# Optimization experiments

Hardware: AMD Instinct MI355X
Metric: run time of the kernel (lower is better)

## Reference

```python
import jax, jax.numpy as jnp
import numpy as np

DIM = 172
MULT = 4
HEADS = 1
B, H, W = 2, 256, 256


def _ln(x, g, b):
    # LayerNorm over last dim, eps=1e-5 (torch default)
    m = jnp.mean(x, axis=-1, keepdims=True)
    v = jnp.mean((x - m) ** 2, axis=-1, keepdims=True)
    return (x - m) * jax.lax.rsqrt(v + 1e-5) * g + b


def _l2norm(x):
    # F.normalize(p=2, dim=-1): x / max(||x||, 1e-12)
    n = jnp.sqrt(jnp.sum(x * x, axis=-1, keepdims=True))
    return x / jnp.maximum(n, 1e-12)


def _gelu(x):
    return jax.nn.gelu(x, approximate=False)


def _dwconv3(x, w):
    # x: [B,C,H,W], w: [C,1,3,3], groups=C, padding=1
    return jax.lax.conv_general_dilated(
        x, w, window_strides=(1, 1), padding='SAME',
        feature_group_count=x.shape[1],
        dimension_numbers=('NCHW', 'OIHW', 'NCHW'))


def _c1x1(x, w):
    # 1x1 conv, no bias. x: [B,I,H,W], w: [O,I,1,1]
    return jnp.einsum('bihw,oi->bohw', x, w[:, :, 0, 0])


def _ms_msa(x, Wq, Wk, Wv, rescale, proj_w, proj_b, pos_w1, pos_w2):
    # x: [b,h,w,c] (already layer-normed)
    b, h, w, c = x.shape
    d = c // HEADS
    n = h * w
    xf = x.reshape(b, n, c)
    q_inp = xf @ Wq.T
    k_inp = xf @ Wk.T
    v_inp = xf @ Wv.T

    def split(t):  # -> [b, heads, d, n]  (b n (h d) -> b h n d, then transpose(-2,-1))
        return t.reshape(b, n, HEADS, d).transpose(0, 2, 3, 1)

    q, k, v = split(q_inp), split(k_inp), split(v_inp)
    q = _l2norm(q)
    k = _l2norm(k)
    attn = jnp.einsum('bhdn,bhen->bhde', k, q)  # k @ q^T -> [b,heads,d,d]
    attn = attn * rescale                        # learnable per-head rescale
    attn = jax.nn.softmax(attn, axis=-1)
    xo = jnp.einsum('bhde,bhen->bhdn', attn, v)  # [b,heads,d,n]
    xo = xo.transpose(0, 3, 1, 2).reshape(b, n, HEADS * d)
    out_c = (xo @ proj_w.T + proj_b).reshape(b, h, w, c)
    # residual positional embedding: depthwise conv -> GELU -> depthwise conv on v_inp
    vim = v_inp.reshape(b, h, w, c).transpose(0, 3, 1, 2)
    out_p = _dwconv3(_gelu(_dwconv3(vim, pos_w1)), pos_w2).transpose(0, 2, 3, 1)
    return out_c + out_p


def _ffn(x, w1, dw, w2):
    # FeedForward: 1x1 expand -> GELU -> 3x3 depthwise -> GELU -> 1x1 project
    y = x.transpose(0, 3, 1, 2)
    y = _gelu(_c1x1(y, w1))
    y = _gelu(_dwconv3(y, dw))
    y = _c1x1(y, w2)
    return y.transpose(0, 2, 3, 1)


def reference(x, ln1_g, ln1_b, Wq, Wk, Wv, rescale, proj_w, proj_b,
              pos_w1, pos_w2, ln2_g, ln2_b, ff_w1, ff_dw, ff_w2):
    # SMSAB forward, num_blocks=1. x: [b,c,h,w]
    y = x.transpose(0, 2, 3, 1)  # [b,h,w,c]
    y = _ms_msa(_ln(y, ln1_g, ln1_b), Wq, Wk, Wv, rescale,
                proj_w, proj_b, pos_w1, pos_w2) + y
    y = _ffn(_ln(y, ln2_g, ln2_b), ff_w1, ff_dw, ff_w2) + y
    return y.transpose(0, 3, 1, 2)  # [b,c,h,w]


def setup_inputs() -> dict:
    key = jax.random.key(0)
    ks = jax.random.split(key, 9)
    s = 0.02
    c, m = DIM, DIM * MULT
    return {
        'x': jax.random.normal(ks[0], (B, c, H, W), jnp.float32),
        'ln1_g': jnp.ones((c,), jnp.float32),
        'ln1_b': jnp.zeros((c,), jnp.float32),
        'Wq': jax.random.normal(ks[1], (c, c), jnp.float32) * s,
        'Wk': jax.random.normal(ks[2], (c, c), jnp.float32) * s,
        'Wv': jax.random.normal(ks[3], (c, c), jnp.float32) * s,
        'rescale': jnp.ones((HEADS, 1, 1), jnp.float32),
        'proj_w': jax.random.normal(ks[4], (c, c), jnp.float32) * s,
        'proj_b': jnp.zeros((c,), jnp.float32),
        'pos_w1': jax.random.normal(ks[5], (c, 1, 3, 3), jnp.float32) * s,
        'pos_w2': jax.random.normal(ks[6], (c, 1, 3, 3), jnp.float32) * s,
        'ln2_g': jnp.ones((c,), jnp.float32),
        'ln2_b': jnp.zeros((c,), jnp.float32),
        'ff_w1': jax.random.normal(ks[7], (m, c, 1, 1), jnp.float32) * s,
        'ff_dw': jax.random.normal(ks[8], (m, 1, 3, 3), jnp.float32) * s,
        'ff_w2': jax.random.normal(jax.random.fold_in(key, 99), (c, m, 1, 1), jnp.float32) * s,
    }
```

## Files before the change

### kernel.cpp

```cpp
#include <hip/hip_runtime.h>
#include <hip/hip_bf16.h>

#define NPIX 65536
#define CP 176
#define EP 704
#define HCC 32

typedef long long i64;
typedef __attribute__((ext_vector_type(8))) short bf8v;
typedef __attribute__((ext_vector_type(8))) float f8v;
typedef __attribute__((ext_vector_type(4))) float f4v;

__device__ __forceinline__ float b2f(unsigned short u) {
  return __uint_as_float(((unsigned)u) << 16);
}
__device__ __forceinline__ short f2b(float v) {
  __hip_bfloat16 h = __float2bfloat16(v);
  return *reinterpret_cast<short*>(&h);
}
__device__ __forceinline__ float ldf(const void* p, i64 i, int bf) {
  return bf ? b2f(((const unsigned short*)p)[i]) : ((const float*)p)[i];
}
__device__ __forceinline__ float gelu_f(float x) {
  float y = 0.7978845608f * (x + 0.044715f * x * x * x);
  float t = 1.f - 2.f / (__expf(2.f * y) + 1.f);
  return 0.5f * x * (1.f + t);
}
__device__ __forceinline__ bf8v ldbf8(const short* p) { return *(const bf8v*)p; }

__global__ void detect_k(const void* g, int* flag) {
  unsigned u = *(const unsigned*)g;
  *flag = (u == 0x3F800000u) ? 0 : 1;
}

__global__ __launch_bounds__(256) void prep_k(
    const void* Wv, const void* fw1, const void* fw2, const void* Wq,
    const void* posw1, const void* posw2, const void* fdw,
    const void* pb, const void* ln2g, const void* ln2b,
    short* Wvb, short* fw1b, short* fw2b, float* Wqt,
    float* p1f, float* p2f, float* fdwf, float* pbf, float* gf, float* bfv,
    float* Gf, const int* flagp)
{
  const int flag = *flagp;
  const int bx = blockIdx.x, t = threadIdx.x;
  switch (blockIdx.y) {
    case 0: {
      if (t < 176) Wvb[(i64)bx * 176 + t] =
        f2b((bx < 172 && t < 172) ? ldf(Wv, (i64)bx * 172 + t, flag) : 0.f);
    } break;
    case 1: {
      if (t < 176)
        for (int m = bx; m < 704; m += 176)
          fw1b[(i64)m * 176 + t] =
            f2b((m < 688 && t < 172) ? ldf(fw1, (i64)m * 172 + t, flag) : 0.f);
    } break;
    case 2: {
      for (int k = t; k < 704; k += 256)
        fw2b[(i64)bx * 704 + k] =
          f2b((bx < 172 && k < 688) ? ldf(fw2, (i64)bx * 688 + k, flag) : 0.f);
    } break;
    case 3: {
      if (t < 176) Wqt[(i64)bx * 176 + t] =
        (bx < 172 && t < 172) ? ldf(Wq, (i64)t * 172 + bx, flag) : 0.f;
    } break;
    case 4: {
      if (bx < 9 && t < 176) p1f[bx * 176 + t] = (t < 172) ? ldf(posw1, (i64)t * 9 + bx, flag) : 0.f;
    } break;
    case 5: {
      if (bx < 9 && t < 176) p2f[bx * 176 + t] = (t < 172) ? ldf(posw2, (i64)t * 9 + bx, flag) : 0.f;
    } break;
    case 6: {
      if (bx < 9)
        for (int c = t; c < 704; c += 256)
          fdwf[bx * 704 + c] = (c < 688) ? ldf(fdw, (i64)c * 9 + bx, flag) : 0.f;
    } break;
    case 7: {
      if (bx == 0 && t < 176) {
        pbf[t] = (t < 172) ? ldf(pb, t, flag) : 0.f;
        gf[t]  = (t < 172) ? ldf(ln2g, t, flag) : 0.f;
        bfv[t] = (t < 172) ? ldf(ln2b, t, flag) : 0.f;
      }
    } break;
    default: {
      for (int i = bx * 256 + t; i < 2 * 176 * 176; i += 176 * 256) Gf[i] = 0.f;
    } break;
  }
}

__global__ __launch_bounds__(256) void ln1_k(const void* __restrict__ x,
    const void* __restrict__ g, const void* __restrict__ bv,
    short* __restrict__ A1, const int* __restrict__ flagp)
{
  const int flag = *flagp;
  __shared__ float gs[176], bs[176];
  __shared__ float part[64][9];
  const int tid = threadIdx.x;
  if (tid < 176) {
    gs[tid] = (tid < 172) ? ldf(g, tid, flag) : 0.f;
    bs[tid] = (tid < 172) ? ldf(bv, tid, flag) : 0.f;
  }
  const int w = tid >> 6, l = tid & 63;
  const i64 gp = (i64)blockIdx.x * 64 + l;
  const int b = (int)(gp >> 16); const i64 n = gp & 65535;
  const i64 xb = (i64)b * 172 * NPIX + n;
  const bf8v z = {0, 0, 0, 0, 0, 0, 0, 0};
  bf8v keep[6];
  float s = 0.f, s2 = 0.f;
  #pragma unroll
  for (int i = 0; i < 6; ++i) {
    int c8 = w + i * 4;
    bf8v t = z;
    if (c8 < 22) {
      #pragma unroll
      for (int j = 0; j < 8; ++j) {
        int c = c8 * 8 + j;
        float v = 0.f;
        if (c < 172) { v = ldf(x, xb + (i64)c * NPIX, flag); s += v; s2 += v * v; }
        t[j] = f2b(v);
      }
    }
    keep[i] = t;
  }
  part[l][w * 2] = s; part[l][w * 2 + 1] = s2;
  __syncthreads();
  float S  = part[l][0] + part[l][2] + part[l][4] + part[l][6];
  float S2 = part[l][1] + part[l][3] + part[l][5] + part[l][7];
  float m = S * (1.f / 172.f);
  float rstd = rsqrtf(S2 * (1.f / 172.f) - m * m + 1e-5f);
  #pragma unroll
  for (int i = 0; i < 6; ++i) {
    int c8 = w + i * 4;
    if (c8 < 22) {
      bf8v t = keep[i], o;
      #pragma unroll
      for (int j = 0; j < 8; ++j) {
        int c = c8 * 8 + j;
        float y = (c < 172) ? (b2f((unsigned short)t[j]) - m) * rstd * gs[c] + bs[c] : 0.f;
        o[j] = f2b(y);
      }
      *(bf8v*)(A1 + gp * 176 + c8 * 8) = o;
    }
  }
}

__global__ __launch_bounds__(256) void gg_k(const short* __restrict__ A1,
                                            float* __restrict__ Gf)
{
  __shared__ short tile[176 * 136];
  const int tid = threadIdx.x;
  const int w = tid >> 6, l = tid & 63, lm = l & 15, ld = l >> 4;
  const int b = blockIdx.y;
  const int row = tid & 127, h = tid >> 7;
  const bf8v z = {0, 0, 0, 0, 0, 0, 0, 0};

  f4v acc[3][11];
  #pragma unroll
  for (int i = 0; i < 3; ++i)
    #pragma unroll
    for (int f = 0; f < 11; ++f) acc[i][f] = f4v{0.f, 0.f, 0.f, 0.f};

  for (int sub = 0; sub < 4; ++sub) {
    __syncthreads();
    const i64 nbase = (i64)blockIdx.x * 512 + sub * 128;
    const short* src = A1 + ((i64)b * NPIX + nbase + row) * 176 + h * 88;
    #pragma unroll
    for (int i = 0; i < 11; ++i) {
      bf8v v = ldbf8(src + i * 8);
      int c0 = h * 88 + i * 8;
      #pragma unroll
      for (int j = 0; j < 8; ++j) tile[(c0 + j) * 136 + row] = v[j];
    }
    __syncthreads();
    #pragma unroll
    for (int ks = 0; ks < 4; ++ks) {
      const int ko = ks * 32 + ld * 8;
      bf8v av[3], bv[11];
      #pragma unroll
      for (int i = 0; i < 3; ++i) {
        int fd = w + i * 4;
        av[i] = (fd < 11) ? *(const bf8v*)&tile[(fd * 16 + lm) * 136 + ko] : z;
      }
      #pragma unroll
      for (int f = 0; f < 11; ++f)
        bv[f] = *(const bf8v*)&tile[(f * 16 + lm) * 136 + ko];
      #pragma unroll
      for (int i = 0; i < 3; ++i)
        #pragma unroll
        for (int f = 0; f < 11; ++f)
          acc[i][f] = __builtin_amdgcn_mfma_f32_16x16x32_bf16(av[i], bv[f], acc[i][f], 0, 0, 0);
    }
  }
  #pragma unroll
  for (int i = 0; i < 3; ++i) {
    int fd = w + i * 4;
    if (fd >= 11) continue;
    #pragma unroll
    for (int f = 0; f < 11; ++f)
      #pragma unroll
      for (int r = 0; r < 4; ++r) {
        int d = fd * 16 + ld * 4 + r;
        int e = f * 16 + lm;
        atomicAdd(Gf + ((i64)b * 176 + d) * 176 + e, acc[i][f][r]);
      }
  }
}

__global__ __launch_bounds__(256) void attn_k1(const float* __restrict__ Gf,
    const void* __restrict__ Wk, const void* __restrict__ Wq,
    float* __restrict__ T, float* __restrict__ invk, float* __restrict__ invq,
    const int* __restrict__ flagp)
{
  const int flag = *flagp;
  const int d = blockIdx.x, b = blockIdx.y, e = threadIdx.x;
  const float* G = Gf + (i64)b * 176 * 176;
  float t = 0.f, tq = 0.f;
  if (e < 176) {
    for (int c = 0; c < 172; ++c) {
      float g = G[(i64)c * 176 + e];
      t  += ldf(Wk, (i64)d * 172 + c, flag) * g;
      tq += ldf(Wq, (i64)d * 172 + c, flag) * g;
    }
    T[((i64)b * 176 + d) * 176 + e] = t;
  }
  float pk = (e < 172) ? t  * ldf(Wk, (i64)d * 172 + e, flag) : 0.f;
  float pq = (e < 172) ? tq * ldf(Wq, (i64)d * 172 + e, flag) : 0.f;
  __shared__ float r1[256], r2[256];
  r1[e] = pk; r2[e] = pq; __syncthreads();
  for (int st = 128; st > 0; st >>= 1) {
    if (e < st) { r1[e] += r1[e + st]; r2[e] += r2[e + st]; }
    __syncthreads();
  }
  if (e == 0) {
    invk[b * 176 + d] = 1.f / fmaxf(sqrtf(fmaxf(r1[0], 0.f)), 1e-12f);
    invq[b * 176 + d] = 1.f / fmaxf(sqrtf(fmaxf(r2[0], 0.f)), 1e-12f);
  }
}

__global__ __launch_bounds__(256) void attn_k2(const float* __restrict__ T,
    const float* __restrict__ Wqt, const float* __restrict__ invk,
    const float* __restrict__ invq, const void* __restrict__ resc,
    float* __restrict__ attnf, const int* __restrict__ flagp)
{
  const int flag = *flagp;
  const int d = blockIdx.x, b = blockIdx.y, e = threadIdx.x;
  __shared__ float tl[176];
  const float* Trow = T + ((i64)b * 176 + d) * 176;
  if (e < 176) tl[e] = Trow[e];
  __syncthreads();
  float val = -1e30f;
  if (e < 172) {
    float a = 0.f;
    for (int c = 0; c < 172; ++c) a += tl[c] * Wqt[(i64)c * 176 + e];
    val = a * invk[b * 176 + d] * invq[b * 176 + e] * ldf(resc, 0, flag);
  }
  __shared__ float red[256];
  red[e] = val; __syncthreads();
  for (int st = 128; st > 0; st >>= 1) {
    if (e < st) red[e] = fmaxf(red[e], red[e + st]);
    __syncthreads();
  }
  float mx = red[0]; __syncthreads();
  float ex = (e < 172) ? __expf(val - mx) : 0.f;
  red[e] = ex; __syncthreads();
  for (int st = 128; st > 0; st >>= 1) {
    if (e < st) red[e] += red[e + st];
    __syncthreads();
  }
  float sm = red[0];
  if (e < 176) attnf[((i64)b * 176 + d) * 176 + e] = (e < 172) ? ex / sm : 0.f;
}

__global__ __launch_bounds__(256) void attn_k3(const float* __restrict__ attnf,
    const void* __restrict__ pw, short* __restrict__ Mb, const int* __restrict__ flagp)
{
  const int flag = *flagp;
  const int o = blockIdx.x, b = blockIdx.y, e = threadIdx.x;
  if (e >= 176) return;
  float m = 0.f;
  if (o < 172 && e < 172)
    for (int d = 0; d < 172; ++d)
      m += ldf(pw, (i64)o * 172 + d, flag) * attnf[((i64)b * 176 + d) * 176 + e];
  Mb[((i64)b * CP + o) * CP + e] = f2b(m);
}

__global__ __launch_bounds__(256) void ffn1_k(
    const short* __restrict__ A1,
    const short* __restrict__ fw1b,
    const float* __restrict__ fdwf,
    short* __restrict__ F, i64 fbs,
    int y0glob)
{
  __shared__ short ering[3][256][HCC];
  __shared__ float wl[9][HCC];
  const int tid = threadIdx.x;
  const int w = tid >> 6, l = tid & 63, lm = l & 15, ld = l >> 4;
  const int hc0 = blockIdx.x * HCC;
  const int b = blockIdx.z;
  const int yb0 = y0glob + blockIdx.y * 8;
  for (int i = tid; i < 9 * HCC; i += 256)
    wl[i / HCC][i % HCC] = fdwf[(i / HCC) * EP + hc0 + (i % HCC)];

  const short* Wl = fw1b + (i64)(hc0 + lm) * CP + ld * 8;
  const bf8v z = {0, 0, 0, 0, 0, 0, 0, 0};

  for (int yy = yb0 - 1; yy <= yb0 + 8; ++yy) {
    const int slot = (yy - (yb0 - 1)) % 3;
    __syncthreads();
    if (yy >= 0 && yy < 256) {
      const i64 prow = (i64)b * NPIX + (i64)yy * 256;
      const short* Xbase = A1 + prow * CP;
      f4v acc[2][4];
      #pragma unroll
      for (int m = 0; m < 2; ++m)
        #pragma unroll
        for (int nt = 0; nt < 4; ++nt) acc[m][nt] = f4v{0.f, 0.f, 0.f, 0.f};
      #pragma unroll
      for (int ks = 0; ks < 6; ++ks) {
        const int ko = ks * 32;
        const bool ok = (ks < 5) || (ld < 2);
        bf8v av[4], bv[2];
        #pragma unroll
        for (int nt = 0; nt < 4; ++nt) {
          const int px0 = (w * 4 + nt) * 16;
          av[nt] = ok ? ldbf8(Xbase + (i64)(px0 + lm) * CP + ld * 8 + ko) : z;
        }
        #pragma unroll
        for (int m = 0; m < 2; ++m)
          bv[m] = ok ? ldbf8(Wl + (i64)m * 16 * CP + ko) : z;
        #pragma unroll
        for (int m = 0; m < 2; ++m)
          #pragma unroll
          for (int nt = 0; nt < 4; ++nt)
            acc[m][nt] = __builtin_amdgcn_mfma_f32_16x16x32_bf16(av[nt], bv[m], acc[m][nt], 0, 0, 0);
      }
      #pragma unroll
      for (int m = 0; m < 2; ++m)
        #pragma unroll
        for (int nt = 0; nt < 4; ++nt) {
          const int px0 = (w * 4 + nt) * 16;
          #pragma unroll
          for (int r = 0; r < 4; ++r)
            ering[slot][px0 + ld * 4 + r][m * 16 + lm] = f2b(gelu_f(acc[m][nt][r]));
        }
    } else {
      bf8v* ep = (bf8v*)&ering[slot][0][0];
      for (int i = tid; i < 256 * HCC / 8; i += 256) ep[i] = z;
    }
    __syncthreads();
    const int fy = yy - 1;
    if (fy >= yb0 && fy <= yb0 + 7) {
      #pragma unroll
      for (int it = 0; it < 4; ++it) {
        const int item = tid + it * 256;
        const int px = item >> 2, g = item & 3;
        float a8[8] = {0.f, 0.f, 0.f, 0.f, 0.f, 0.f, 0.f, 0.f};
        #pragma unroll
        for (int dy = -1; dy <= 1; ++dy) {
          const int sl = (fy + dy - yb0 + 1) % 3;
          #pragma unroll
          for (int dx = -1; dx <= 1; ++dx) {
            const int xx = px + dx;
            if (xx < 0 || xx > 255) continue;
            bf8v v = *(const bf8v*)&ering[sl][xx][g * 8];
            const float* wp = &wl[(dy + 1) * 3 + (dx + 1)][g * 8];
            #pragma unroll
            for (int j = 0; j < 8; ++j) a8[j] += b2f((unsigned short)v[j]) * wp[j];
          }
        }
        bf8v o;
        #pragma unroll
        for (int j = 0; j < 8; ++j) o[j] = f2b(gelu_f(a8[j]));
        const i64 frow = (i64)(fy - y0glob) * 256 + px;
        *(bf8v*)(F + b * fbs + frow * (i64)EP + hc0 + g * 8) = o;
      }
    }
  }
}

template<int MODE, bool GELU_>
__global__ __launch_bounds__(256) void gemm_k(
    const short* __restrict__ Wb, i64 wbs,
    const short* __restrict__ X, i64 xbs, int Kp,
    const float* __restrict__ bias,
    const short* __restrict__ add0, i64 a0bs,
    const void* __restrict__ xres,
    void* __restrict__ outp, i64 obs, int ocols, i64 out_n0,
    short* __restrict__ Y1,
    const float* __restrict__ gf, const float* __restrict__ bfv,
    const int* __restrict__ flagp)
{
  __shared__ short tl[(MODE >= 2) ? 4 * 32 * 176 : 1];
  __shared__ float2 stt[(MODE == 3) ? 4 * 32 : 1];
  const int tid = threadIdx.x;
  const int w = tid >> 6, l = tid & 63;
  const int lm = l & 15, ld = l >> 4;
  const int b = blockIdx.z;
  const int co0 = blockIdx.y * CP;
  const i64 nloc = (i64)blockIdx.x * 128 + w * 32;

  const short* Xl = X + b * xbs + (nloc + lm) * (i64)Kp + ld * 8;
  const short* Wl = Wb + b * wbs + (i64)(co0 + lm) * Kp + ld * 8;

  f4v acc[2][11];
  #pragma unroll
  for (int a = 0; a < 2; ++a)
    #pragma unroll
    for (int f = 0; f < 11; ++f) acc[a][f] = f4v{0.f, 0.f, 0.f, 0.f};

  const int nfull = Kp >> 5;
  for (int s = 0; s < nfull; ++s) {
    const int ko = s * 32;
    bf8v av0 = ldbf8(Xl + ko);
    bf8v av1 = ldbf8(Xl + (i64)16 * Kp + ko);
    bf8v bv[11];
    #pragma unroll
    for (int f = 0; f < 11; ++f) bv[f] = ldbf8(Wl + (i64)f * 16 * Kp + ko);
    #pragma unroll
    for (int f = 0; f < 11; ++f) {
      acc[0][f] = __builtin_amdgcn_mfma_f32_16x16x32_bf16(av0, bv[f], acc[0][f], 0, 0, 0);
      acc[1][f] = __builtin_amdgcn_mfma_f32_16x16x32_bf16(av1, bv[f], acc[1][f], 0, 0, 0);
    }
  }
  if (Kp & 31) {
    const int ko = nfull * 32;
    const bf8v z = {0, 0, 0, 0, 0, 0, 0, 0};
    const bool ok = (ld < 2);
    bf8v av0 = ok ? ldbf8(Xl + ko) : z;
    bf8v av1 = ok ? ldbf8(Xl + (i64)16 * Kp + ko) : z;
    bf8v bv[11];
    #pragma unroll
    for (int f = 0; f < 11; ++f) bv[f] = ok ? ldbf8(Wl + (i64)f * 16 * Kp + ko) : z;
    #pragma unroll
    for (int f = 0; f < 11; ++f) {
      acc[0][f] = __builtin_amdgcn_mfma_f32_16x16x32_bf16(av0, bv[f], acc[0][f], 0, 0, 0);
      acc[1][f] = __builtin_amdgcn_mfma_f32_16x16x32_bf16(av1, bv[f], acc[1][f], 0, 0, 0);
    }
  }

  const int flag = (MODE >= 2) ? *flagp : 0;

  if (MODE == 0) {
    #pragma unroll
    for (int a = 0; a < 2; ++a)
      #pragma unroll
      for (int f = 0; f < 11; ++f) {
        const int col = co0 + f * 16 + lm;
        #pragma unroll
        for (int r = 0; r < 4; ++r) {
          float v = acc[a][f][r];
          if (GELU_) v = gelu_f(v);
          const i64 row = nloc + a * 16 + ld * 4 + r;
          ((short*)outp)[b * obs + row * ocols + col] = f2b(v);
        }
      }
  } else if (MODE == 2) {
    #pragma unroll
    for (int a = 0; a < 2; ++a)
      #pragma unroll
      for (int f = 0; f < 11; ++f) {
        const int col = co0 + f * 16 + lm;
        #pragma unroll
        for (int r = 0; r < 4; ++r) {
          const int row32 = a * 16 + ld * 4 + r;
          tl[(w * 32 + row32) * 176 + col] = f2b(acc[a][f][r]);
        }
      }
    #pragma unroll
    for (int cc = 0; cc < 3; ++cc) {
      const int col = l + cc * 64;
      if (col < 172) {
        const i64 gn = out_n0 + nloc;
        bf8v vv[4], yv[4];
        #pragma unroll
        for (int i = 0; i < 4; ++i)
          #pragma unroll
          for (int j = 0; j < 8; ++j)
            vv[i][j] = tl[(w * 32 + i * 8 + j) * 176 + col];
        const short* yp = Y1 + ((i64)b * CP + col) * NPIX + gn;
        #pragma unroll
        for (int i = 0; i < 4; ++i) yv[i] = ldbf8(yp + i * 8);
        if (flag) {
          short* op = (short*)outp + ((i64)b * 172 + col) * NPIX + gn;
          #pragma unroll
          for (int i = 0; i < 4; ++i) {
            bf8v ov;
            #pragma unroll
            for (int j = 0; j < 8; ++j)
              ov[j] = f2b(b2f((unsigned short)vv[i][j]) + b2f((unsigned short)yv[i][j]));
            *(bf8v*)(op + i * 8) = ov;
          }
        } else {
          float* op = (float*)outp + ((i64)b * 172 + col) * NPIX + gn;
          #pragma unroll
          for (int i = 0; i < 4; ++i) {
            f8v fo;
            #pragma unroll
            for (int j = 0; j < 8; ++j)
              fo[j] = b2f((unsigned short)vv[i][j]) + b2f((unsigned short)yv[i][j]);
            *(f8v*)(op + i * 8) = fo;
          }
        }
      }
    }
  } else {
    #pragma unroll
    for (int a = 0; a < 2; ++a)
      #pragma unroll
      for (int f = 0; f < 11; ++f) {
        const int col = co0 + f * 16 + lm;
        const float bvl = bias ? bias[col] : 0.f;
        #pragma unroll
        for (int r = 0; r < 4; ++r) {
          float v = acc[a][f][r] + bvl;
          const int row32 = a * 16 + ld * 4 + r;
          const i64 row = nloc + row32;
          v += b2f(((const unsigned short*)add0)[b * a0bs + row * ocols + col]);
          tl[(w * 32 + row32) * 176 + col] = f2b(v);
        }
      }
    #pragma unroll
    for (int cc = 0; cc < 3; ++cc) {
      const int col = l + cc * 64;
      if (col < 172) {
        bf8v vv[4];
        #pragma unroll
        for (int i = 0; i < 4; ++i)
          #pragma unroll
          for (int j = 0; j < 8; ++j)
            vv[i][j] = tl[(w * 32 + i * 8 + j) * 176 + col];
        const i64 xoff = ((i64)b * 172 + col) * NPIX + nloc;
        if (flag) {
          #pragma unroll
          for (int i = 0; i < 4; ++i) {
            bf8v xv = ldbf8((const short*)xres + xoff + i * 8);
            #pragma unroll
            for (int j = 0; j < 8; ++j)
              vv[i][j] = f2b(b2f((unsigned short)vv[i][j]) + b2f((unsigned short)xv[j]));
          }
        } else {
          const float* xp = (const float*)xres + xoff;
          #pragma unroll
          for (int i = 0; i < 4; ++i) {
            f8v xv = *(const f8v*)(xp + i * 8);
            #pragma unroll
            for (int j = 0; j < 8; ++j)
              vv[i][j] = f2b(b2f((unsigned short)vv[i][j]) + xv[j]);
          }
        }
        short* yp = Y1 + ((i64)b * CP + col) * NPIX + nloc;
        #pragma unroll
        for (int i = 0; i < 4; ++i) {
          #pragma unroll
          for (int j = 0; j < 8; ++j)
            tl[(w * 32 + i * 8 + j) * 176 + col] = vv[i][j];
          *(bf8v*)(yp + i * 8) = vv[i];
        }
      }
    }
    {
      const int p = l >> 1, h = l & 1;
      float s_ = 0.f, q_ = 0.f;
      #pragma unroll
      for (int ii = 0; ii < 11; ++ii) {
        bf8v v = *(const bf8v*)&tl[(w * 32 + p) * 176 + (h * 11 + ii) * 8];
        #pragma unroll
        for (int j = 0; j < 8; ++j) { float t = b2f((unsigned short)v[j]); s_ += t; q_ += t * t; }
      }
      s_ += __shfl_xor(s_, 1); q_ += __shfl_xor(q_, 1);
      if (h == 0) {
        float mean = s_ * (1.f / 172.f);
        float rstd = rsqrtf(q_ * (1.f / 172.f) - mean * mean + 1e-5f);
        stt[w * 32 + p] = make_float2(mean, rstd);
      }
    }
    #pragma unroll
    for (int ii = 0; ii < 11; ++ii) {
      const int ch = l + ii * 64;
      const int p = ch / 22, g = ch % 22;
      float2 st = stt[w * 32 + p];
      f8v gv = *(const f8v*)(gf + g * 8);
      f8v bv2 = *(const f8v*)(bfv + g * 8);
      bf8v v = *(const bf8v*)&tl[(w * 32 + p) * 176 + g * 8];
      bf8v o;
      #pragma unroll
      for (int j = 0; j < 8; ++j)
        o[j] = f2b((b2f((unsigned short)v[j]) - st.x) * st.y * gv[j] + bv2[j]);
      *(bf8v*)((short*)outp + b * obs + (nloc + p) * (i64)ocols + g * 8) = o;
    }
  }
}

template<int RC, bool GELU_>
__global__ __launch_bounds__(256) void dwc_k(const short* __restrict__ in, i64 ibs,
    int iy0, const float* __restrict__ wf,
    short* __restrict__ out, i64 obs, int oy0)
{
  constexpr int Cp = RC * 8;
  __shared__ float wl[9 * Cp];
  for (int i = threadIdx.x; i < 9 * Cp; i += 256) wl[i] = wf[i];
  __syncthreads();
  const int b = blockIdx.z;
  const int yl = blockIdx.y;
  const int yg = oy0 + yl;
  const int cir = blockIdx.x * 256 + threadIdx.x;
  const int x = cir / RC, g = cir % RC;
  float acc[8] = {0.f, 0.f, 0.f, 0.f, 0.f, 0.f, 0.f, 0.f};
  #pragma unroll
  for (int dy = -1; dy <= 1; ++dy) {
    const int yy = yg + dy;
    if (yy < 0 || yy > 255) continue;
    const short* rp = in + b * ibs + (i64)(yy - iy0) * (256 * RC) * 8;
    #pragma unroll
    for (int dx = -1; dx <= 1; ++dx) {
      const int xx = x + dx;
      if (xx < 0 || xx > 255) continue;
      bf8v v = ldbf8(rp + (i64)(cir + dx * RC) * 8);
      const float* wp = wl + ((dy + 1) * 3 + (dx + 1)) * Cp + g * 8;
      #pragma unroll
      for (int j = 0; j < 8; ++j) acc[j] += b2f((unsigned short)v[j]) * wp[j];
    }
  }
  bf8v o;
  #pragma unroll
  for (int j = 0; j < 8; ++j) o[j] = f2b(GELU_ ? gelu_f(acc[j]) : acc[j]);
  *(bf8v*)(out + b * obs + ((i64)yl * (256 * RC) + cir) * 8) = o;
}

extern "C" void kernel_launch(void* const* d_in, const int* in_sizes, int n_in,
                              void* d_out, int out_size, void* d_ws, size_t ws_size,
                              hipStream_t stream)
{
  const void* x     = d_in[0];
  const void* ln1g  = d_in[1];
  const void* ln1b  = d_in[2];
  const void* Wq    = d_in[3];
  const void* Wk    = d_in[4];
  const void* Wv    = d_in[5];
  const void* resc  = d_in[6];
  const void* pw    = d_in[7];
  const void* pb    = d_in[8];
  const void* posw1 = d_in[9];
  const void* posw2 = d_in[10];
  const void* ln2g  = d_in[11];
  const void* ln2b  = d_in[12];
  const void* fw1   = d_in[13];
  const void* fdw   = d_in[14];
  const void* fw2   = d_in[15];

  char* ws = (char*)d_ws;
  size_t off = 0;
  auto alloc = [&](size_t bytes) {
    void* p = ws + off;
    off = (off + bytes + 255) & ~(size_t)255;
    return p;
  };
  int*    flagp = (int*)   alloc(16);
  float*  invq  = (float*) alloc(2 * 176 * 4);
  float*  invk  = (float*) alloc(2 * 176 * 4);
  float*  Gf    = (float*) alloc((size_t)2 * 176 * 176 * 4);
  float*  Tf    = (float*) alloc((size_t)2 * 176 * 176 * 4);
  float*  attnf = (float*) alloc((size_t)2 * 176 * 176 * 4);
  short*  Mb    = (short*) alloc((size_t)2 * CP * CP * 2);
  float*  Wqt   = (float*) alloc((size_t)176 * 176 * 4);
  short*  Wvb   = (short*) alloc((size_t)CP * CP * 2);
  short*  fw1b  = (short*) alloc((size_t)EP * CP * 2);
  short*  fw2b  = (short*) alloc((size_t)CP * EP * 2);
  float*  p1f   = (float*) alloc((size_t)9 * CP * 4);
  float*  p2f   = (float*) alloc((size_t)9 * CP * 4);
  float*  fdwf  = (float*) alloc((size_t)9 * EP * 4);
  float*  pbf   = (float*) alloc((size_t)CP * 4);
  float*  gf    = (float*) alloc((size_t)CP * 4);
  float*  bfv   = (float*) alloc((size_t)CP * 4);
  const size_t BUF = (size_t)2 * NPIX * CP * 2;
  short* A1 = (short*)alloc(BUF);
  short* Yb = (short*)alloc(BUF);
  short* D  = (short*)alloc(BUF);
  short* P2 = (short*)alloc(BUF);
  alloc(4 * 1024 * 1024);
  if (off > ws_size) return;

  const i64 CBS  = (i64)NPIX * CP;
  const i64 FBS2 = (i64)32768 * EP;
  short* F = D;

  detect_k<<<1, 1, 0, stream>>>(ln1g, flagp);

  prep_k<<<dim3(176, 9), 256, 0, stream>>>(Wv, fw1, fw2, Wq, posw1, posw2, fdw,
      pb, ln2g, ln2b, Wvb, fw1b, fw2b, Wqt, p1f, p2f, fdwf, pbf, gf, bfv,
      Gf, flagp);

  ln1_k<<<2048, 256, 0, stream>>>(x, ln1g, ln1b, A1, flagp);

  gg_k<<<dim3(128, 2), 256, 0, stream>>>(A1, Gf);
  attn_k1<<<dim3(172, 2), 256, 0, stream>>>(Gf, Wk, Wq, Tf, invk, invq, flagp);
  attn_k2<<<dim3(172, 2), 256, 0, stream>>>(Tf, Wqt, invk, invq, resc, attnf, flagp);
  attn_k3<<<dim3(176, 2), 256, 0, stream>>>(attnf, pw, Mb, flagp);

  gemm_k<0, false><<<dim3(512, 1, 2), 256, 0, stream>>>(
      Wvb, 0, A1, CBS, CP, nullptr, nullptr, 0, nullptr,
      D, CBS, CP, 0, nullptr, nullptr, nullptr, flagp);

  dwc_k<22, true ><<<dim3(22, 256, 2), 256, 0, stream>>>(D,  CBS, 0, p1f, Yb, CBS, 0);
  dwc_k<22, false><<<dim3(22, 256, 2), 256, 0, stream>>>(Yb, CBS, 0, p2f, P2, CBS, 0);

  gemm_k<3, false><<<dim3(512, 1, 2), 256, 0, stream>>>(
      Mb, (i64)CP * CP, D, CBS, CP, pbf, P2, CBS, x,
      A1, CBS, CP, 0, Yb, gf, bfv, flagp);

  for (int ci = 0; ci < 2; ++ci) {
    ffn1_k<<<dim3(22, 16, 2), 256, 0, stream>>>(
        A1, fw1b, fdwf, F, FBS2, ci * 128);
    gemm_k<2, false><<<dim3(256, 1, 2), 256, 0, stream>>>(
        fw2b, 0, F, FBS2, EP, nullptr, nullptr, 0, nullptr,
        d_out, 0, 0, (i64)ci * 32768, Yb, nullptr, nullptr, flagp);
  }
}
```

Measured before the change: 881.7 us.

## Halve ffn1 channel tile, keep fp32 padded row ring in shared memory

The fused expand-GEMM plus depthwise kernel now handles 16 hidden channels per block instead of 32, which doubles the grid. Its three-row ring buffer holds fp32 values with zero-padded halo columns, so the 3x3 stencil no longer needs bounds checks or bf16 conversions. The goal is more blocks in flight and a cheaper stencil inner loop. In exchange, each block reloads the same input activation rows for only half the output channels, doubling A1 reads and lowering MFMA reuse per load.

Result: slower. 952.8 us (+8.1%).

```diff
diff --git a/kernel.cpp b/kernel.cpp
--- a/kernel.cpp
+++ b/kernel.cpp
@@ -4,7 +4,7 @@
 #define NPIX 65536
 #define CP 176
 #define EP 704
-#define HCC 32
+#define HCC 16
 
 typedef long long i64;
 typedef __attribute__((ext_vector_type(8))) short bf8v;
@@ -290,15 +290,19 @@
     short* __restrict__ F, i64 fbs,
     int y0glob)
 {
-  __shared__ short ering[3][256][HCC];
+  __shared__ __attribute__((aligned(32))) float ering[3][258][HCC];
   __shared__ float wl[9][HCC];
   const int tid = threadIdx.x;
   const int w = tid >> 6, l = tid & 63, lm = l & 15, ld = l >> 4;
   const int hc0 = blockIdx.x * HCC;
   const int b = blockIdx.z;
   const int yb0 = y0glob + blockIdx.y * 8;
-  for (int i = tid; i < 9 * HCC; i += 256)
-    wl[i / HCC][i % HCC] = fdwf[(i / HCC) * EP + hc0 + (i % HCC)];
+  if (tid < 9 * HCC)
+    wl[tid / HCC][tid % HCC] = fdwf[(tid / HCC) * EP + hc0 + (tid % HCC)];
+  if (tid < 3 * 2 * HCC) {
+    const int sl = tid / (2 * HCC), rest = tid % (2 * HCC);
+    ering[sl][(rest < HCC) ? 0 : 257][rest % HCC] = 0.f;
+  }
 
   const short* Wl = fw1b + (i64)(hc0 + lm) * CP + ld * 8;
   const bf8v z = {0, 0, 0, 0, 0, 0, 0, 0};
@@ -309,62 +313,52 @@
     if (yy >= 0 && yy < 256) {
       const i64 prow = (i64)b * NPIX + (i64)yy * 256;
       const short* Xbase = A1 + prow * CP;
-      f4v acc[2][4];
-      #pragma unroll
-      for (int m = 0; m < 2; ++m)
-        #pragma unroll
-        for (int nt = 0; nt < 4; ++nt) acc[m][nt] = f4v{0.f, 0.f, 0.f, 0.f};
+      f4v acc[4];
+      #pragma unroll
+      for (int nt = 0; nt < 4; ++nt) acc[nt] = f4v{0.f, 0.f, 0.f, 0.f};
       #pragma unroll
       for (int ks = 0; ks < 6; ++ks) {
         const int ko = ks * 32;
         const bool ok = (ks < 5) || (ld < 2);
-        bf8v av[4], bv[2];
+        bf8v av[4];
         #pragma unroll
         for (int nt = 0; nt < 4; ++nt) {
           const int px0 = (w * 4 + nt) * 16;
           av[nt] = ok ? ldbf8(Xbase + (i64)(px0 + lm) * CP + ld * 8 + ko) : z;
         }
-        #pragma unroll
-        for (int m = 0; m < 2; ++m)
-          bv[m] = ok ? ldbf8(Wl + (i64)m * 16 * CP + ko) : z;
-        #pragma unroll
-        for (int m = 0; m < 2; ++m)
-          #pragma unroll
-          for (int nt = 0; nt < 4; ++nt)
-            acc[m][nt] = __builtin_amdgcn_mfma_f32_16x16x32_bf16(av[nt], bv[m], acc[m][nt], 0, 0, 0);
-      }
-      #pragma unroll
-      for (int m = 0; m < 2; ++m)
-        #pragma unroll
-        for (int nt = 0; nt < 4; ++nt) {
-          const int px0 = (w * 4 + nt) * 16;
-          #pragma unroll
-          for (int r = 0; r < 4; ++r)
-            ering[slot][px0 + ld * 4 + r][m * 16 + lm] = f2b(gelu_f(acc[m][nt][r]));
-        }
+        bf8v bv = ok ? ldbf8(Wl + ko) : z;
+        #pragma unroll
+        for (int nt = 0; nt < 4; ++nt)
+          acc[nt] = __builtin_amdgcn_mfma_f32_16x16x32_bf16(av[nt], bv, acc[nt], 0, 0, 0);
+      }
+      #pragma unroll
+      for (int nt = 0; nt < 4; ++nt) {
+        const int px0 = (w * 4 + nt) * 16;
+        #pragma unroll
+        for (int r = 0; r < 4; ++r)
+          ering[slot][1 + px0 + ld * 4 + r][lm] = gelu_f(acc[nt][r]);
+      }
     } else {
-      bf8v* ep = (bf8v*)&ering[slot][0][0];
-      for (int i = tid; i < 256 * HCC / 8; i += 256) ep[i] = z;
+      for (int i = tid; i < 256 * HCC; i += 256)
+        ering[slot][1 + i / HCC][i % HCC] = 0.f;
     }
     __syncthreads();
     const int fy = yy - 1;
     if (fy >= yb0 && fy <= yb0 + 7) {
       #pragma unroll
-      for (int it = 0; it < 4; ++it) {
+      for (int it = 0; it < 2; ++it) {
         const int item = tid + it * 256;
-        const int px = item >> 2, g = item & 3;
+        const int px = item >> 1, g = item & 1;
         float a8[8] = {0.f, 0.f, 0.f, 0.f, 0.f, 0.f, 0.f, 0.f};
         #pragma unroll
         for (int dy = -1; dy <= 1; ++dy) {
           const int sl = (fy + dy - yb0 + 1) % 3;
           #pragma unroll
           for (int dx = -1; dx <= 1; ++dx) {
-            const int xx = px + dx;
-            if (xx < 0 || xx > 255) continue;
-            bf8v v = *(const bf8v*)&ering[sl][xx][g * 8];
+            f8v v = *(const f8v*)&ering[sl][1 + px + dx][g * 8];
             const float* wp = &wl[(dy + 1) * 3 + (dx + 1)][g * 8];
             #pragma unroll
-            for (int j = 0; j < 8; ++j) a8[j] += b2f((unsigned short)v[j]) * wp[j];
+            for (int j = 0; j < 8; ++j) a8[j] += v[j] * wp[j];
           }
         }
         bf8v o;
@@ -708,7 +702,7 @@
       A1, CBS, CP, 0, Yb, gf, bfv, flagp);
 
   for (int ci = 0; ci < 2; ++ci) {
-    ffn1_k<<<dim3(22, 16, 2), 256, 0, stream>>>(
+    ffn1_k<<<dim3(44, 16, 2), 256, 0, stream>>>(
         A1, fw1b, fdwf, F, FBS2, ci * 128);
     gemm_k<2, false><<<dim3(256, 1, 2), 256, 0, stream>>>(
         fw2b, 0, F, FBS2, EP, nullptr, nullptr, 0, nullptr,
```
